# Kernel tuning notes

Hardware: AMD Instinct MI355X
Metric: run time of the kernel (lower is better)

The kernel has to match this reference:

```python
import jax, jax.numpy as jnp
import numpy as np

NUM_EXPERTS = 8
TOP_K = 2
HIDDEN = 768
INTERMEDIATE = 3072
NUM_TOKENS = 8192


def setup_inputs() -> dict:
    key = jax.random.key(0)
    k0, k1, k2, k3 = jax.random.split(key, 4)
    hidden_states = jax.random.normal(k0, (NUM_TOKENS, HIDDEN), dtype=jnp.float32)
    router_weight = jax.random.normal(k1, (NUM_EXPERTS, HIDDEN), dtype=jnp.float32) * 0.02
    w1 = jax.random.normal(k2, (NUM_EXPERTS, INTERMEDIATE, HIDDEN), dtype=jnp.float32) * 0.02
    w2 = jax.random.normal(k3, (NUM_EXPERTS, HIDDEN, INTERMEDIATE), dtype=jnp.float32) * 0.02
    bias = jnp.zeros((HIDDEN,), dtype=jnp.float32)
    return {"hidden_states": hidden_states, "router_weight": router_weight,
            "w1": w1, "w2": w2, "bias": bias}


def _moe_forward(hidden_states, router_weight, w1, w2, bias):
    T, H = hidden_states.shape
    E = w1.shape[0]
    # Router: ReplicatedLinear(H, E, bias=False)
    logits = hidden_states @ router_weight.T                      # [T, E]
    # fused_topk: softmax over all experts, then top-k, renormalize=False
    probs = jax.nn.softmax(logits, axis=-1)                       # [T, E]
    topk_w, topk_ids = jax.lax.top_k(probs, TOP_K)                # [T, K]
    # per-token per-expert combine weight (top-k ids are distinct)
    gates = jnp.sum(jax.nn.one_hot(topk_ids, E, dtype=probs.dtype) * topk_w[..., None], axis=1)  # [T, E]
    # Expert MLP: y_e = gelu(x @ w1[e].T) @ w2[e].T  (non-gated, activation_without_mul('gelu'))
    out = jnp.zeros_like(hidden_states)
    for e in range(E):  # small fixed expert count
        h = jax.nn.gelu(hidden_states @ w1[e].T, approximate=False)  # [T, I]
        out = out + gates[:, e:e + 1] * (h @ w2[e].T)                # [T, H]
    return out + bias


def reference(hidden_states, router_weight, w1, w2, bias):
    return _moe_forward(hidden_states, router_weight, w1, w2, bias)
```

## Files before the change

### kernel.cpp

```cpp
#include <hip/hip_runtime.h>
#include <hip/hip_bf16.h>
#include <math.h>

#define NT 8192
#define HD 768
#define ID 3072
#define NE 8
#define BK 32
#define MAXB1 136
#define MAXB2 72
#define ASZ1 (128 * BK)
#define ASZ2 (256 * BK)
#define BSZ  (128 * BK)

typedef __bf16 bf16x8 __attribute__((ext_vector_type(8)));
typedef float f32x4 __attribute__((ext_vector_type(4)));

__device__ __forceinline__ unsigned short f2bf(float f) {
    union { float f; unsigned u; } v; v.f = f;
    unsigned r = v.u + 0x7FFFu + ((v.u >> 16) & 1u);
    return (unsigned short)(r >> 16);
}
__device__ __forceinline__ float bf2f(unsigned short b) {
    union { unsigned u; float f; } v; v.u = ((unsigned)b) << 16;
    return v.f;
}
__device__ __forceinline__ float gelu_t(float v) {
    float u = 0.7978845608028654f * (v + 0.044715f * v * v * v);
    float t = __expf(-2.0f * fabsf(u));
    float th = (1.0f - t) / (1.0f + t);
    return 0.5f * v * (1.0f + copysignf(th, u));
}

__device__ __forceinline__ void gload16(const void* g, void* l) {
    auto* lds = reinterpret_cast<__attribute__((address_space(3))) unsigned int*>(
        reinterpret_cast<uintptr_t>(l));
    auto* gp = reinterpret_cast<const __attribute__((address_space(1))) unsigned int*>(
        reinterpret_cast<uintptr_t>(g));
    __builtin_amdgcn_global_load_lds(gp, lds, 16, 0, 0);
}

__global__ void k_convertw(const float4* __restrict__ w1, const float4* __restrict__ w2,
                           ushort4* __restrict__ w1b, ushort4* __restrict__ w2b, int n) {
    int i = blockIdx.x * 256 + threadIdx.x;
    if (i >= n) return;
    float4 a = w1[i]; float4 b = w2[i];
    ushort4 ra, rb;
    ra.x = f2bf(a.x); ra.y = f2bf(a.y); ra.z = f2bf(a.z); ra.w = f2bf(a.w);
    rb.x = f2bf(b.x); rb.y = f2bf(b.y); rb.z = f2bf(b.z); rb.w = f2bf(b.w);
    w1b[i] = ra; w2b[i] = rb;
}

__global__ void k_router(const float* __restrict__ x, const float* __restrict__ rw,
                         ushort4* __restrict__ xb4, float* __restrict__ gates,
                         uchar2* __restrict__ choice) {
    __shared__ float rws[NE * HD];
    const int tid = threadIdx.x;
    for (int i = tid; i < NE * HD / 4; i += 256)
        ((float4*)rws)[i] = ((const float4*)rw)[i];
    __syncthreads();
    const int wid = tid >> 6, lane = tid & 63;
    const float4* rws4 = (const float4*)rws;
    for (int it = 0; it < 8; ++it) {
        const int t = blockIdx.x * 32 + wid * 8 + it;
        const float4* xp4 = (const float4*)(x + (size_t)t * HD);
        float acc[NE];
#pragma unroll
        for (int e = 0; e < NE; e++) acc[e] = 0.f;
#pragma unroll
        for (int j = 0; j < HD / 256; j++) {
            float4 v = xp4[lane + 64 * j];
            ushort4 o;
            o.x = f2bf(v.x); o.y = f2bf(v.y); o.z = f2bf(v.z); o.w = f2bf(v.w);
            xb4[(size_t)t * (HD / 4) + lane + 64 * j] = o;
#pragma unroll
            for (int e = 0; e < NE; e++) {
                float4 w = rws4[e * (HD / 4) + lane + 64 * j];
                acc[e] += v.x * w.x + v.y * w.y + v.z * w.z + v.w * w.w;
            }
        }
#pragma unroll
        for (int e = 0; e < NE; e++)
            for (int off = 32; off; off >>= 1) acc[e] += __shfl_xor(acc[e], off);
        if (lane == 0) {
            float mx = acc[0];
#pragma unroll
            for (int e = 1; e < NE; e++) mx = fmaxf(mx, acc[e]);
            float p[NE], s = 0.f;
#pragma unroll
            for (int e = 0; e < NE; e++) { p[e] = __expf(acc[e] - mx); s += p[e]; }
            float inv = 1.f / s;
            int i1 = 0; float b1 = p[0];
#pragma unroll
            for (int e = 1; e < NE; e++) if (p[e] > b1) { b1 = p[e]; i1 = e; }
            int i2 = (i1 == 0) ? 1 : 0; float b2 = p[i2];
#pragma unroll
            for (int e = 0; e < NE; e++) if (e != i1 && p[e] > b2) { b2 = p[e]; i2 = e; }
            choice[t].x = (unsigned char)i1;
            choice[t].y = (unsigned char)i2;
            gates[2 * t] = b1 * inv;
            gates[2 * t + 1] = b2 * inv;
        }
    }
}

__global__ void k_scatter(const uchar2* __restrict__ choice,
                          int* __restrict__ lists, int* __restrict__ counts) {
    const int e = blockIdx.x;
    const int tid = threadIdx.x, wid = tid >> 6, lane = tid & 63;
    __shared__ int wtot[4];
    __shared__ int running;
    if (tid == 0) running = 0;
    __syncthreads();
    for (int t0 = 0; t0 < NT; t0 += 256) {
        const int t = t0 + tid;
        uchar2 c = choice[t];
        bool m1 = (c.x == e), m2 = (c.y == e);
        bool m = m1 || m2;
        int slot = m1 ? 2 * t : 2 * t + 1;
        unsigned long long mask = __ballot(m);
        int off = __popcll(mask & ((1ULL << lane) - 1ULL));
        if (lane == 0) wtot[wid] = __popcll(mask);
        __syncthreads();
        int base = running;
        for (int w = 0; w < wid; w++) base += wtot[w];
        if (m) lists[e * NT + base + off] = slot;
        __syncthreads();
        if (tid == 0) running += wtot[0] + wtot[1] + wtot[2] + wtot[3];
        __syncthreads();
    }
    if (tid == 0) counts[e] = running;
}

__global__ void k_plan(const int* __restrict__ counts,
                       int2* __restrict__ table1, int2* __restrict__ table2) {
    __shared__ int s1[NE + 1], s2[NE + 1];
    const int tid = threadIdx.x;
    if (tid == 0) {
        int a = 0, b = 0;
        for (int e = 0; e < NE; e++) {
            s1[e] = a; a += (counts[e] + 127) >> 7;
            s2[e] = b; b += (counts[e] + 255) >> 8;
        }
        s1[NE] = a; s2[NE] = b;
    }
    __syncthreads();
    for (int b = tid; b < MAXB1; b += 256) {
        int e = -1, m0 = 0;
#pragma unroll
        for (int q = 0; q < NE; q++)
            if (b >= s1[q] && b < s1[q + 1]) { e = q; m0 = (b - s1[q]) << 7; }
        table1[b].x = e; table1[b].y = m0;
    }
    for (int b = tid; b < MAXB2; b += 256) {
        int e = -1, m0 = 0;
#pragma unroll
        for (int q = 0; q < NE; q++)
            if (b >= s2[q] && b < s2[q + 1]) { e = q; m0 = (b - s2[q]) << 8; }
        table2[b].x = e; table2[b].y = m0;
    }
}


__launch_bounds__(256, 3)
__global__ void k_gemm1(const unsigned short* __restrict__ xb, const unsigned short* __restrict__ w1b,
                        const int* __restrict__ lists, const int* __restrict__ counts,
                        const int2* __restrict__ table,
                        unsigned short* __restrict__ hbuf) {
    const int2 ent = table[(blockIdx.x & 7) * (MAXB1 >> 3) + (blockIdx.x >> 3)];
    const int e = ent.x;
    if (e < 0) return;
    const int m0 = ent.y;
    const int cnt = counts[e];
    const int n0 = blockIdx.y * 128;
    __shared__ __align__(16) unsigned short As[3 * ASZ1];
    __shared__ __align__(16) unsigned short Bs[3 * BSZ];
    __shared__ int slot_s[128];
    const int tid = threadIdx.x, lane = tid & 63, wid = tid >> 6;
    if (tid < 128) {
        int r = m0 + tid;
        slot_s[tid] = lists[e * NT + (r < cnt ? r : cnt - 1)];
    }
    __syncthreads();

    const int rsub = lane >> 2;
    const int sw = (((lane & 3) ^ ((rsub >> 1) & 3)) * 8);
    const int row0 = wid * 16 + rsub;
    const unsigned short* gA0 = xb + (size_t)(slot_s[row0] >> 1) * HD + sw;
    const unsigned short* gA1 = xb + (size_t)(slot_s[row0 + 64] >> 1) * HD + sw;
    const unsigned short* gB0 = w1b + ((size_t)e * ID + n0 + row0) * HD + sw;
    const unsigned short* gB1 = gB0 + (size_t)64 * HD;
    auto stage = [&](int bf) {
        gload16(gA0, As + bf * ASZ1 + wid * 512);       gA0 += BK;
        gload16(gA1, As + bf * ASZ1 + (wid + 4) * 512); gA1 += BK;
        gload16(gB0, Bs + bf * BSZ + wid * 512);        gB0 += BK;
        gload16(gB1, Bs + bf * BSZ + (wid + 4) * 512);  gB1 += BK;
    };

    const int wr = wid >> 1, wc = wid & 1;
    const int l15 = lane & 15, l4 = lane >> 4;
    const int aBase = (wr * 64 + l15) * BK;
    const int bBase = (wc * 64 + l15) * BK;
    const int cs = (l4 ^ ((l15 >> 1) & 3)) * 8;

    f32x4 acc[4][4];
    f32x4 zero = {0.f, 0.f, 0.f, 0.f};
#pragma unroll
    for (int m = 0; m < 4; m++)
#pragma unroll
        for (int n = 0; n < 4; n++) acc[m][n] = zero;

    const int NK = HD / BK;
    stage(0); stage(1);
    int cur = 0, pf = 2;
    for (int kt = 0; kt < NK; ++kt) {
        if (kt + 1 < NK) asm volatile("s_waitcnt vmcnt(4)\ns_barrier" ::: "memory");
        else             asm volatile("s_waitcnt vmcnt(0)\ns_barrier" ::: "memory");
        if (kt + 2 < NK) { stage(pf); pf = (pf == 2) ? 0 : pf + 1; }
        const unsigned short* Ab = As + cur * ASZ1;
        const unsigned short* Bb = Bs + cur * BSZ;
        bf16x8 a[4], b[4];
#pragma unroll
        for (int m = 0; m < 4; m++) a[m] = *(const bf16x8*)(Ab + aBase + m * 512 + cs);
#pragma unroll
        for (int n = 0; n < 4; n++) b[n] = *(const bf16x8*)(Bb + bBase + n * 512 + cs);
#pragma unroll
        for (int m = 0; m < 4; m++)
#pragma unroll
            for (int n = 0; n < 4; n++)
                acc[m][n] = __builtin_amdgcn_mfma_f32_16x16x32_bf16(a[m], b[n], acc[m][n], 0, 0, 0);
        cur = (cur == 2) ? 0 : cur + 1;
    }
    const int rj = l4 * 4;
#pragma unroll
    for (int m = 0; m < 4; m++) {
#pragma unroll
        for (int j = 0; j < 4; j++) {
            int lr2 = wr * 64 + m * 16 + rj + j;
            if (m0 + lr2 < cnt) {
                int slot = slot_s[lr2];
                size_t rowoff = (size_t)slot * ID + n0 + wc * 64 + l15;
#pragma unroll
                for (int n = 0; n < 4; n++)
                    hbuf[rowoff + n * 16] = f2bf(gelu_t(acc[m][n][j]));
            }
        }
    }
}

__launch_bounds__(512, 2)
__global__ void k_gemm2(const unsigned short* __restrict__ hbuf, const unsigned short* __restrict__ w2b,
                        const int* __restrict__ lists, const int* __restrict__ counts,
                        const int2* __restrict__ table,
                        const float* __restrict__ gates, unsigned short* __restrict__ pout) {
    const int2 ent = table[(blockIdx.x & 7) * (MAXB2 >> 3) + (blockIdx.x >> 3)];
    const int e = ent.x;
    if (e < 0) return;
    const int m0 = ent.y;
    const int cnt = counts[e];
    const int n0 = blockIdx.y * 128;
    __shared__ __align__(16) unsigned short As[3 * ASZ2];
    __shared__ __align__(16) unsigned short Bs[3 * BSZ];
    __shared__ int slot_s[256];
    const int tid = threadIdx.x, lane = tid & 63, wid = tid >> 6;
    if (tid < 256) {
        int r = m0 + tid;
        slot_s[tid] = lists[e * NT + (r < cnt ? r : cnt - 1)];
    }
    __syncthreads();

    const int rsub = lane >> 2;
    const int sw = (((lane & 3) ^ ((rsub >> 1) & 3)) * 8);
    const unsigned short* gA[2];
#pragma unroll
    for (int i = 0; i < 2; i++) {
        int row = wid * 16 + rsub + 128 * i;
        gA[i] = hbuf + (size_t)slot_s[row] * ID + sw;
    }
    const unsigned short* gB = w2b + ((size_t)e * HD + n0 + wid * 16 + rsub) * ID + sw;
    auto stage = [&](int bf) {
#pragma unroll
        for (int i = 0; i < 2; i++) { gload16(gA[i], As + bf * ASZ2 + (wid + 8 * i) * 512); gA[i] += BK; }
        gload16(gB, Bs + bf * BSZ + wid * 512); gB += BK;
    };

    const int wr = wid >> 1, wc = wid & 1;
    const int l15 = lane & 15, l4 = lane >> 4;
    const int aBase = (wr * 64 + l15) * BK;
    const int bBase = (wc * 64 + l15) * BK;
    const int cs = (l4 ^ ((l15 >> 1) & 3)) * 8;

    f32x4 acc[4][4];
    f32x4 zero = {0.f, 0.f, 0.f, 0.f};
#pragma unroll
    for (int m = 0; m < 4; m++)
#pragma unroll
        for (int n = 0; n < 4; n++) acc[m][n] = zero;

    const int NK = ID / BK;
    stage(0); stage(1);
    int cur = 0, pf = 2;
    for (int kt = 0; kt < NK; ++kt) {
        if (kt + 1 < NK) asm volatile("s_waitcnt vmcnt(3)\ns_barrier" ::: "memory");
        else             asm volatile("s_waitcnt vmcnt(0)\ns_barrier" ::: "memory");
        if (kt + 2 < NK) { stage(pf); pf = (pf == 2) ? 0 : pf + 1; }
        const unsigned short* Ab = As + cur * ASZ2;
        const unsigned short* Bb = Bs + cur * BSZ;
        bf16x8 a[4], b[4];
#pragma unroll
        for (int m = 0; m < 4; m++) a[m] = *(const bf16x8*)(Ab + aBase + m * 512 + cs);
#pragma unroll
        for (int n = 0; n < 4; n++) b[n] = *(const bf16x8*)(Bb + bBase + n * 512 + cs);
#pragma unroll
        for (int m = 0; m < 4; m++)
#pragma unroll
            for (int n = 0; n < 4; n++)
                acc[m][n] = __builtin_amdgcn_mfma_f32_16x16x32_bf16(a[m], b[n], acc[m][n], 0, 0, 0);
        cur = (cur == 2) ? 0 : cur + 1;
    }
    const int rj = l4 * 4;
#pragma unroll
    for (int m = 0; m < 4; m++) {
#pragma unroll
        for (int j = 0; j < 4; j++) {
            int lr2 = wr * 64 + m * 16 + rj + j;
            if (m0 + lr2 < cnt) {
                int slot = slot_s[lr2];
                float g = gates[slot];
                size_t rowoff = (size_t)slot * HD + n0 + wc * 64 + l15;
#pragma unroll
                for (int n = 0; n < 4; n++)
                    pout[rowoff + n * 16] = f2bf(g * acc[m][n][j]);
            }
        }
    }
}

__global__ void k_combine(const unsigned short* __restrict__ pout, const float* __restrict__ bias,
                          float4* __restrict__ out) {
    int idx = blockIdx.x * 256 + threadIdx.x;
    int t = idx / (HD / 4);
    int c = idx - t * (HD / 4);
    ushort4 a = ((const ushort4*)pout)[(size_t)t * (2 * HD / 4) + c];
    ushort4 b = ((const ushort4*)pout)[(size_t)t * (2 * HD / 4) + HD / 4 + c];
    float4 bb = ((const float4*)bias)[c];
    float4 r;
    r.x = bf2f(a.x) + bf2f(b.x) + bb.x;
    r.y = bf2f(a.y) + bf2f(b.y) + bb.y;
    r.z = bf2f(a.z) + bf2f(b.z) + bb.z;
    r.w = bf2f(a.w) + bf2f(b.w) + bb.w;
    out[idx] = r;
}

extern "C" void kernel_launch(void* const* d_in, const int* in_sizes, int n_in,
                              void* d_out, int out_size, void* d_ws, size_t ws_size,
                              hipStream_t stream) {
    const float* x    = (const float*)d_in[0];
    const float* rw   = (const float*)d_in[1];
    const float* w1   = (const float*)d_in[2];
    const float* w2   = (const float*)d_in[3];
    const float* bias = (const float*)d_in[4];
    float* out = (float*)d_out;

    char* ws = (char*)d_ws;
    size_t off = 0;
    auto alloc = [&](size_t bytes) -> char* {
        char* p = ws + off;
        off += (bytes + 255) & ~(size_t)255;
        return p;
    };
    int*            counts = (int*)alloc(NE * 4);
    int2*           table1 = (int2*)alloc(MAXB1 * sizeof(int2));
    int2*           table2 = (int2*)alloc(MAXB2 * sizeof(int2));
    int*            lists  = (int*)alloc((size_t)NE * NT * 4);
    float*          gates  = (float*)alloc((size_t)NT * 2 * 4);
    uchar2*         choice = (uchar2*)alloc((size_t)NT * 2);
    unsigned short* xb     = (unsigned short*)alloc((size_t)NT * HD * 2);
    unsigned short* w1b    = (unsigned short*)alloc((size_t)NE * ID * HD * 2);
    unsigned short* w2b    = (unsigned short*)alloc((size_t)NE * HD * ID * 2);
    unsigned short* hbuf   = (unsigned short*)alloc((size_t)NT * 2 * ID * 2);
    unsigned short* pout   = (unsigned short*)alloc((size_t)NT * 2 * HD * 2);

    const int n4 = NE * ID * HD / 4;
    k_convertw<<<dim3((n4 + 255) / 256), dim3(256), 0, stream>>>(
        (const float4*)w1, (const float4*)w2, (ushort4*)w1b, (ushort4*)w2b, n4);
    k_router<<<dim3(NT / 32), dim3(256), 0, stream>>>(x, rw, (ushort4*)xb, gates, choice);
    k_scatter<<<dim3(NE), dim3(256), 0, stream>>>(choice, lists, counts);
    k_plan<<<dim3(1), dim3(256), 0, stream>>>(counts, table1, table2);
    k_gemm1<<<dim3(MAXB1, ID / 128), dim3(256), 0, stream>>>(xb, w1b, lists, counts, table1, hbuf);
    k_gemm2<<<dim3(MAXB2, HD / 128), dim3(512), 0, stream>>>(hbuf, w2b, lists, counts, table2, gates, pout);
    k_combine<<<dim3(NT * HD / 4 / 256), dim3(256), 0, stream>>>(pout, bias, (float4*)out);
}
```

Before: 309.7 us.

## Fuse weight conversion into router, inline plan, swap MFMA operands for packed stores

```diff
diff --git a/kernel.cpp b/kernel.cpp
--- a/kernel.cpp
+++ b/kernel.cpp
@@ -12,6 +12,8 @@
 #define ASZ1 (128 * BK)
 #define ASZ2 (256 * BK)
 #define BSZ  (128 * BK)
+#define RT_BLOCKS (NT / 32)
+#define CONV_BLOCKS (NE * ID * HD / 4 / 256)
 
 typedef __bf16 bf16x8 __attribute__((ext_vector_type(8)));
 typedef float f32x4 __attribute__((ext_vector_type(4)));
@@ -25,11 +27,10 @@
     union { unsigned u; float f; } v; v.u = ((unsigned)b) << 16;
     return v.f;
 }
-__device__ __forceinline__ float gelu_t(float v) {
-    float u = 0.7978845608028654f * (v + 0.044715f * v * v * v);
-    float t = __expf(-2.0f * fabsf(u));
-    float th = (1.0f - t) / (1.0f + t);
-    return 0.5f * v * (1.0f + copysignf(th, u));
+__device__ __forceinline__ float gelu_s(float v) {
+    float z = v * (1.5957691216057308f + 0.07135481283687945f * v * v);
+    float e = __expf(-z);
+    return v * __builtin_amdgcn_rcpf(1.0f + e);
 }
 
 __device__ __forceinline__ void gload16(const void* g, void* l) {
@@ -40,22 +41,22 @@
     __builtin_amdgcn_global_load_lds(gp, lds, 16, 0, 0);
 }
 
-__global__ void k_convertw(const float4* __restrict__ w1, const float4* __restrict__ w2,
-                           ushort4* __restrict__ w1b, ushort4* __restrict__ w2b, int n) {
-    int i = blockIdx.x * 256 + threadIdx.x;
-    if (i >= n) return;
-    float4 a = w1[i]; float4 b = w2[i];
-    ushort4 ra, rb;
-    ra.x = f2bf(a.x); ra.y = f2bf(a.y); ra.z = f2bf(a.z); ra.w = f2bf(a.w);
-    rb.x = f2bf(b.x); rb.y = f2bf(b.y); rb.z = f2bf(b.z); rb.w = f2bf(b.w);
-    w1b[i] = ra; w2b[i] = rb;
-}
-
-__global__ void k_router(const float* __restrict__ x, const float* __restrict__ rw,
-                         ushort4* __restrict__ xb4, float* __restrict__ gates,
-                         uchar2* __restrict__ choice) {
+__global__ void k_front(const float* __restrict__ x, const float* __restrict__ rw,
+                        const float4* __restrict__ w1, const float4* __restrict__ w2,
+                        ushort4* __restrict__ w1b, ushort4* __restrict__ w2b,
+                        ushort4* __restrict__ xb4, float* __restrict__ gates,
+                        uchar2* __restrict__ choice) {
     __shared__ float rws[NE * HD];
     const int tid = threadIdx.x;
+    if (blockIdx.x >= RT_BLOCKS) {
+        int i = (blockIdx.x - RT_BLOCKS) * 256 + tid;
+        float4 a = w1[i]; float4 b = w2[i];
+        ushort4 ra, rb;
+        ra.x = f2bf(a.x); ra.y = f2bf(a.y); ra.z = f2bf(a.z); ra.w = f2bf(a.w);
+        rb.x = f2bf(b.x); rb.y = f2bf(b.y); rb.z = f2bf(b.z); rb.w = f2bf(b.w);
+        w1b[i] = ra; w2b[i] = rb;
+        return;
+    }
     for (int i = tid; i < NE * HD / 4; i += 256)
         ((float4*)rws)[i] = ((const float4*)rw)[i];
     __syncthreads();
@@ -132,45 +133,23 @@
     if (tid == 0) counts[e] = running;
 }
 
-__global__ void k_plan(const int* __restrict__ counts,
-                       int2* __restrict__ table1, int2* __restrict__ table2) {
-    __shared__ int s1[NE + 1], s2[NE + 1];
-    const int tid = threadIdx.x;
-    if (tid == 0) {
-        int a = 0, b = 0;
-        for (int e = 0; e < NE; e++) {
-            s1[e] = a; a += (counts[e] + 127) >> 7;
-            s2[e] = b; b += (counts[e] + 255) >> 8;
-        }
-        s1[NE] = a; s2[NE] = b;
-    }
-    __syncthreads();
-    for (int b = tid; b < MAXB1; b += 256) {
-        int e = -1, m0 = 0;
-#pragma unroll
-        for (int q = 0; q < NE; q++)
-            if (b >= s1[q] && b < s1[q + 1]) { e = q; m0 = (b - s1[q]) << 7; }
-        table1[b].x = e; table1[b].y = m0;
-    }
-    for (int b = tid; b < MAXB2; b += 256) {
-        int e = -1, m0 = 0;
-#pragma unroll
-        for (int q = 0; q < NE; q++)
-            if (b >= s2[q] && b < s2[q + 1]) { e = q; m0 = (b - s2[q]) << 8; }
-        table2[b].x = e; table2[b].y = m0;
-    }
-}
-
 
 __launch_bounds__(256, 3)
 __global__ void k_gemm1(const unsigned short* __restrict__ xb, const unsigned short* __restrict__ w1b,
                         const int* __restrict__ lists, const int* __restrict__ counts,
-                        const int2* __restrict__ table,
                         unsigned short* __restrict__ hbuf) {
-    const int2 ent = table[(blockIdx.x & 7) * (MAXB1 >> 3) + (blockIdx.x >> 3)];
-    const int e = ent.x;
+    const int bsw = (blockIdx.x & 7) * (MAXB1 >> 3) + (blockIdx.x >> 3);
+    int e = -1, m0 = 0;
+    {
+        int s = 0;
+#pragma unroll
+        for (int q = 0; q < NE; q++) {
+            int nb = (counts[q] + 127) >> 7;
+            if (bsw >= s && bsw < s + nb) { e = q; m0 = (bsw - s) << 7; }
+            s += nb;
+        }
+    }
     if (e < 0) return;
-    const int m0 = ent.y;
     const int cnt = counts[e];
     const int n0 = blockIdx.y * 128;
     __shared__ __align__(16) unsigned short As[3 * ASZ1];
@@ -228,21 +207,26 @@
         for (int m = 0; m < 4; m++)
 #pragma unroll
             for (int n = 0; n < 4; n++)
-                acc[m][n] = __builtin_amdgcn_mfma_f32_16x16x32_bf16(a[m], b[n], acc[m][n], 0, 0, 0);
+                acc[m][n] = __builtin_amdgcn_mfma_f32_16x16x32_bf16(b[n], a[m], acc[m][n], 0, 0, 0);
         cur = (cur == 2) ? 0 : cur + 1;
     }
     const int rj = l4 * 4;
 #pragma unroll
     for (int m = 0; m < 4; m++) {
-#pragma unroll
-        for (int j = 0; j < 4; j++) {
-            int lr2 = wr * 64 + m * 16 + rj + j;
-            if (m0 + lr2 < cnt) {
-                int slot = slot_s[lr2];
-                size_t rowoff = (size_t)slot * ID + n0 + wc * 64 + l15;
-#pragma unroll
-                for (int n = 0; n < 4; n++)
-                    hbuf[rowoff + n * 16] = f2bf(gelu_t(acc[m][n][j]));
+        int lr2 = wr * 64 + m * 16 + l15;
+        if (m0 + lr2 < cnt) {
+            int slot = slot_s[lr2];
+            unsigned short* hp = hbuf + (size_t)slot * ID + n0 + wc * 64 + rj;
+#pragma unroll
+            for (int n = 0; n < 4; n++) {
+                float g0 = gelu_s(acc[m][n][0]);
+                float g1 = gelu_s(acc[m][n][1]);
+                float g2 = gelu_s(acc[m][n][2]);
+                float g3 = gelu_s(acc[m][n][3]);
+                uint2 pk;
+                pk.x = ((unsigned)f2bf(g1) << 16) | f2bf(g0);
+                pk.y = ((unsigned)f2bf(g3) << 16) | f2bf(g2);
+                *(uint2*)(hp + n * 16) = pk;
             }
         }
     }
@@ -251,12 +235,19 @@
 __launch_bounds__(512, 2)
 __global__ void k_gemm2(const unsigned short* __restrict__ hbuf, const unsigned short* __restrict__ w2b,
                         const int* __restrict__ lists, const int* __restrict__ counts,
-                        const int2* __restrict__ table,
                         const float* __restrict__ gates, unsigned short* __restrict__ pout) {
-    const int2 ent = table[(blockIdx.x & 7) * (MAXB2 >> 3) + (blockIdx.x >> 3)];
-    const int e = ent.x;
+    const int bsw = (blockIdx.x & 7) * (MAXB2 >> 3) + (blockIdx.x >> 3);
+    int e = -1, m0 = 0;
+    {
+        int s = 0;
+#pragma unroll
+        for (int q = 0; q < NE; q++) {
+            int nb = (counts[q] + 255) >> 8;
+            if (bsw >= s && bsw < s + nb) { e = q; m0 = (bsw - s) << 8; }
+            s += nb;
+        }
+    }
     if (e < 0) return;
-    const int m0 = ent.y;
     const int cnt = counts[e];
     const int n0 = blockIdx.y * 128;
     __shared__ __align__(16) unsigned short As[3 * ASZ2];
@@ -315,22 +306,27 @@
         for (int m = 0; m < 4; m++)
 #pragma unroll
             for (int n = 0; n < 4; n++)
-                acc[m][n] = __builtin_amdgcn_mfma_f32_16x16x32_bf16(a[m], b[n], acc[m][n], 0, 0, 0);
+                acc[m][n] = __builtin_amdgcn_mfma_f32_16x16x32_bf16(b[n], a[m], acc[m][n], 0, 0, 0);
         cur = (cur == 2) ? 0 : cur + 1;
     }
     const int rj = l4 * 4;
 #pragma unroll
     for (int m = 0; m < 4; m++) {
-#pragma unroll
-        for (int j = 0; j < 4; j++) {
-            int lr2 = wr * 64 + m * 16 + rj + j;
-            if (m0 + lr2 < cnt) {
-                int slot = slot_s[lr2];
-                float g = gates[slot];
-                size_t rowoff = (size_t)slot * HD + n0 + wc * 64 + l15;
-#pragma unroll
-                for (int n = 0; n < 4; n++)
-                    pout[rowoff + n * 16] = f2bf(g * acc[m][n][j]);
+        int lr2 = wr * 64 + m * 16 + l15;
+        if (m0 + lr2 < cnt) {
+            int slot = slot_s[lr2];
+            float g = gates[slot];
+            unsigned short* pp = pout + (size_t)slot * HD + n0 + wc * 64 + rj;
+#pragma unroll
+            for (int n = 0; n < 4; n++) {
+                float g0 = g * acc[m][n][0];
+                float g1 = g * acc[m][n][1];
+                float g2 = g * acc[m][n][2];
+                float g3 = g * acc[m][n][3];
+                uint2 pk;
+                pk.x = ((unsigned)f2bf(g1) << 16) | f2bf(g0);
+                pk.y = ((unsigned)f2bf(g3) << 16) | f2bf(g2);
+                *(uint2*)(pp + n * 16) = pk;
             }
         }
     }
@@ -370,8 +366,6 @@
         return p;
     };
     int*            counts = (int*)alloc(NE * 4);
-    int2*           table1 = (int2*)alloc(MAXB1 * sizeof(int2));
-    int2*           table2 = (int2*)alloc(MAXB2 * sizeof(int2));
     int*            lists  = (int*)alloc((size_t)NE * NT * 4);
     float*          gates  = (float*)alloc((size_t)NT * 2 * 4);
     uchar2*         choice = (uchar2*)alloc((size_t)NT * 2);
@@ -381,13 +375,11 @@
     unsigned short* hbuf   = (unsigned short*)alloc((size_t)NT * 2 * ID * 2);
     unsigned short* pout   = (unsigned short*)alloc((size_t)NT * 2 * HD * 2);
 
-    const int n4 = NE * ID * HD / 4;
-    k_convertw<<<dim3((n4 + 255) / 256), dim3(256), 0, stream>>>(
-        (const float4*)w1, (const float4*)w2, (ushort4*)w1b, (ushort4*)w2b, n4);
-    k_router<<<dim3(NT / 32), dim3(256), 0, stream>>>(x, rw, (ushort4*)xb, gates, choice);
+    k_front<<<dim3(RT_BLOCKS + CONV_BLOCKS), dim3(256), 0, stream>>>(
+        x, rw, (const float4*)w1, (const float4*)w2,
+        (ushort4*)w1b, (ushort4*)w2b, (ushort4*)xb, gates, choice);
     k_scatter<<<dim3(NE), dim3(256), 0, stream>>>(choice, lists, counts);
-    k_plan<<<dim3(1), dim3(256), 0, stream>>>(counts, table1, table2);
-    k_gemm1<<<dim3(MAXB1, ID / 128), dim3(256), 0, stream>>>(xb, w1b, lists, counts, table1, hbuf);
-    k_gemm2<<<dim3(MAXB2, HD / 128), dim3(512), 0, stream>>>(hbuf, w2b, lists, counts, table2, gates, pout);
+    k_gemm1<<<dim3(MAXB1, ID / 128), dim3(256), 0, stream>>>(xb, w1b, lists, counts, hbuf);
+    k_gemm2<<<dim3(MAXB2, HD / 128), dim3(512), 0, stream>>>(hbuf, w2b, lists, counts, gates, pout);
     k_combine<<<dim3(NT * HD / 4 / 256), dim3(256), 0, stream>>>(pout, bias, (float4*)out);
 }
```

Result: faster. 293.5 us (-5.2%).
